# Kernel optimization log

Measured on AMD Instinct MI355X. Metric: run time of the kernel, lower is better.

The kernel has to match this reference:

```python
import jax, jax.numpy as jnp
import numpy as np

BS = 16384   # batch size
D = 2048     # input_dim
BD = 64      # block_dim
NB = D // BD # 32 blocks per BlockMLP
H = 2 * BD   # hidden block dim (hidden_layers_ratio=[2])
NUM_LAYERS = 2  # ceil(log_64(2048)) = 2


def setup_inputs() -> dict:
    key = jax.random.key(0)
    ks = jax.random.split(key, 1 + 2 * NUM_LAYERS)
    inp = {"x": jax.random.normal(ks[0], (BS, D), dtype=jnp.float32)}
    for i in range(NUM_LAYERS):
        inp[f"W1_{i}"] = jax.random.normal(ks[1 + 2 * i], (NB, BD, H), dtype=jnp.float32)
        inp[f"b1_{i}"] = jnp.zeros((NB, 1, H), dtype=jnp.float32)
        inp[f"W2_{i}"] = jax.random.normal(ks[2 + 2 * i], (NB, H, BD), dtype=jnp.float32)
        inp[f"b2_{i}"] = jnp.zeros((NB, 1, BD), dtype=jnp.float32)
    return inp


def _block_mlp(y, W1, b1, W2, b2):
    # BlockMLP.forward: view(bs, n_blocks, block_dim) -> transpose to [n_blocks, bs, block_dim]
    bs = y.shape[0]
    yb = y.reshape(bs, NB, BD).transpose(1, 0, 2)          # [NB, bs, BD]
    h = jnp.einsum('nbi,nio->nbo', yb, W1) + b1             # [NB, bs, H]
    h = jax.nn.gelu(h, approximate=False)                   # torch nn.GELU default (erf)
    o = jnp.einsum('nbh,nho->nbo', h, W2) + b2              # [NB, bs, BD]
    return o.transpose(1, 0, 2).reshape(bs, -1)             # [bs, D]


def reference(x, W1_0, b1_0, W2_0, b2_0, W1_1, b1_1, W2_1, b2_1):
    bs = x.shape[0]
    params = [(W1_0, b1_0, W2_0, b2_0), (W1_1, b1_1, W2_1, b2_1)]
    y = x
    for i, (W1, b1, W2, b2) in enumerate(params):
        # butterfly-style mixing permute before the block MLP
        y = y.reshape(-1, BD, BD ** i).transpose(0, 2, 1).reshape(bs, -1)
        y = _block_mlp(y, W1, b1, W2, b2)
        # inverse-style permute after
        y = y.reshape(-1, BD ** i, BD).transpose(0, 2, 1)
    return y.reshape(bs, -1)
```

## Files before the change

### kernel.cpp

```cpp
#include <hip/hip_runtime.h>

#define D    2048
#define NB   32
#define BD   64
#define HD   128
#define WSZ  (NB * HD * BD)
#define TSZ  (16384 * 64)

typedef __attribute__((ext_vector_type(8))) short short8;
typedef __attribute__((ext_vector_type(4))) float floatx4;

static __device__ __forceinline__ unsigned short f2bf(float f) {
  union { float f; unsigned u; } v; v.f = f;
  return (unsigned short)((v.u + 0x7FFFu + ((v.u >> 16) & 1u)) >> 16);
}
static __device__ __forceinline__ float bf2f(unsigned short h) {
  union { unsigned u; float f; } v; v.u = ((unsigned)h) << 16;
  return v.f;
}
static __device__ __forceinline__ unsigned fbits(float f) {
  union { float f; unsigned u; } v; v.f = f; return v.u;
}
static __device__ __forceinline__ unsigned short tbf(float f) {
  return (unsigned short)(fbits(f) >> 16);
}
static __device__ __forceinline__ unsigned pkt(float a, float b) {
  return __builtin_amdgcn_perm(fbits(b), fbits(a), 0x07060302u);
}
static __device__ __forceinline__ float fast_exp2(float x) {
  float r; asm("v_exp_f32 %0, %1" : "=v"(r) : "v"(x)); return r;
}
static __device__ __forceinline__ float fast_rcp(float x) {
  float r; asm("v_rcp_f32 %0, %1" : "=v"(r) : "v"(x)); return r;
}
static __device__ __forceinline__ float gelu_f(float x) {
  float x2 = x * x;
  float w  = __builtin_fmaf(x2, -0.102943695f, -2.3022083f);
  float e  = fast_exp2(x * w);
  return x * fast_rcp(1.0f + e);
}

__global__ __launch_bounds__(256, 3) void mlp0_k(
    const float* __restrict__ xf,
    unsigned short* __restrict__ Yt0,
    const unsigned short* __restrict__ Wt1,
    const unsigned short* __restrict__ Wt2,
    const float* __restrict__ b1, const float* __restrict__ b2) {
  __shared__ unsigned short Wlds[16384];
  __shared__ unsigned short Olds[64 * 128];
  __shared__ float Blds[192];
  const int n     = blockIdx.x & 31;
  const int chunk = blockIdx.x >> 5;
  const int t = threadIdx.x, l = t & 63, wv = t >> 6;
  const int lr = l & 15, q = l >> 4;
  const int sw = (lr & 7) << 3;
  const size_t rowbase = (size_t)chunk * 256;

  const unsigned short* s1 = Wt1 + n * 8192;
  const unsigned short* s2 = Wt2 + n * 8192;
  short8 sv1[4], sv2[4];
#pragma unroll
  for (int j = 0; j < 4; ++j) {
    sv1[j] = *(const short8*)&s1[(j * 256 + t) * 8];
    sv2[j] = *(const short8*)&s2[(j * 256 + t) * 8];
  }
  float bv = 0.f;
  if (t < 128)      bv = b1[n * HD + t];
  else if (t < 192) bv = b2[n * BD + (t - 128)];
  float4 uf[2][4];
#pragma unroll
  for (int p = 0; p < 2; ++p) {
    const float* xr = xf + (rowbase + p * 64 + wv * 16 + lr) * D + n * BD + q * 8;
    uf[p][0] = *(const float4*)(xr);      uf[p][1] = *(const float4*)(xr + 4);
    uf[p][2] = *(const float4*)(xr + 32); uf[p][3] = *(const float4*)(xr + 36);
  }
  asm volatile("" ::: "memory");
#pragma unroll
  for (int j = 0; j < 4; ++j) {
    *(short8*)&Wlds[(j * 256 + t) * 8]        = sv1[j];
    *(short8*)&Wlds[8192 + (j * 256 + t) * 8] = sv2[j];
  }
  if (t < 192) Blds[t] = bv;
  __syncthreads();

  const unsigned short* w1p0 = &Wlds[lr * 64 + ((q * 8) ^ sw)];
  const unsigned short* w1p1 = &Wlds[lr * 64 + ((32 + q * 8) ^ sw)];
  const unsigned short* w2p0 = &Wlds[8192 + lr * 128 + ((q * 8) ^ sw)];
  const unsigned short* w2p1 = &Wlds[8192 + lr * 128 + ((32 + q * 8) ^ sw)];

#pragma unroll
  for (int half = 0; half < 2; ++half) {
#pragma unroll
    for (int it = 0; it < 2; ++it) {
      const int i    = half * 2 + it;
      const int slot = i & 1;
      short8 xb0, xb1;
      {
        union { unsigned u[4]; short8 s; } c0, c1;
        c0.u[0] = pkt(uf[slot][0].x, uf[slot][0].y);
        c0.u[1] = pkt(uf[slot][0].z, uf[slot][0].w);
        c0.u[2] = pkt(uf[slot][1].x, uf[slot][1].y);
        c0.u[3] = pkt(uf[slot][1].z, uf[slot][1].w);
        c1.u[0] = pkt(uf[slot][2].x, uf[slot][2].y);
        c1.u[1] = pkt(uf[slot][2].z, uf[slot][2].w);
        c1.u[2] = pkt(uf[slot][3].x, uf[slot][3].y);
        c1.u[3] = pkt(uf[slot][3].z, uf[slot][3].w);
        xb0 = c0.s; xb1 = c1.s;
      }
      if (i < 2) {
        const float* xr = xf + (rowbase + (i + 2) * 64 + wv * 16 + lr) * D + n * BD + q * 8;
        uf[slot][0] = *(const float4*)(xr);      uf[slot][1] = *(const float4*)(xr + 4);
        uf[slot][2] = *(const float4*)(xr + 32); uf[slot][3] = *(const float4*)(xr + 36);
        asm volatile("" ::: "memory");
      }

      floatx4 acc2[4];
#pragma unroll
      for (int ot = 0; ot < 4; ++ot) {
        const float4 bb = *(const float4*)&Blds[128 + ot * 16 + q * 4];
        floatx4 v; v[0] = bb.x; v[1] = bb.y; v[2] = bb.z; v[3] = bb.w;
        acc2[ot] = v;
      }
#pragma unroll
      for (int hf = 0; hf < 2; ++hf) {
        floatx4 acc1[4];
#pragma unroll
        for (int ot = 0; ot < 4; ++ot) {
          const float4 bb = *(const float4*)&Blds[hf * 64 + ot * 16 + q * 4];
          floatx4 v; v[0] = bb.x; v[1] = bb.y; v[2] = bb.z; v[3] = bb.w;
          acc1[ot] = v;
        }
#pragma unroll
        for (int ot = 0; ot < 4; ++ot) {
          const int off = (hf * 64 + ot * 16) * 64;
          short8 a0 = *(const short8*)&w1p0[off];
          short8 a1 = *(const short8*)&w1p1[off];
          acc1[ot] = __builtin_amdgcn_mfma_f32_16x16x32_bf16(a0, xb0, acc1[ot], 0, 0, 0);
          acc1[ot] = __builtin_amdgcn_mfma_f32_16x16x32_bf16(a1, xb1, acc1[ot], 0, 0, 0);
        }
        union { unsigned u[4]; short8 s; } hb0, hb1;
        hb0.u[0] = pkt(gelu_f(acc1[0][0]), gelu_f(acc1[0][1]));
        hb0.u[1] = pkt(gelu_f(acc1[0][2]), gelu_f(acc1[0][3]));
        hb0.u[2] = pkt(gelu_f(acc1[1][0]), gelu_f(acc1[1][1]));
        hb0.u[3] = pkt(gelu_f(acc1[1][2]), gelu_f(acc1[1][3]));
        hb1.u[0] = pkt(gelu_f(acc1[2][0]), gelu_f(acc1[2][1]));
        hb1.u[1] = pkt(gelu_f(acc1[2][2]), gelu_f(acc1[2][3]));
        hb1.u[2] = pkt(gelu_f(acc1[3][0]), gelu_f(acc1[3][1]));
        hb1.u[3] = pkt(gelu_f(acc1[3][2]), gelu_f(acc1[3][3]));
#pragma unroll
        for (int ot = 0; ot < 4; ++ot) {
          const int off = ot * 16 * 128 + hf * 64;
          short8 w0 = *(const short8*)&w2p0[off];
          short8 w1 = *(const short8*)&w2p1[off];
          acc2[ot] = __builtin_amdgcn_mfma_f32_16x16x32_bf16(w0, hb0.s, acc2[ot], 0, 0, 0);
          acc2[ot] = __builtin_amdgcn_mfma_f32_16x16x32_bf16(w1, hb1.s, acc2[ot], 0, 0, 0);
        }
      }
      const int rl = it * 64 + wv * 16 + lr;
#pragma unroll
      for (int ot = 0; ot < 4; ++ot) {
#pragma unroll
        for (int e = 0; e < 4; ++e) {
          const int fo = ot * 16 + q * 4 + e;
          Olds[fo * 128 + (rl ^ ((fo & 7) << 3))] = tbf(acc2[ot][e]);
        }
      }
    }
    __syncthreads();
    const int j = t & 63, w = t >> 6;
#pragma unroll
    for (int ii = 0; ii < 8; ++ii) {
      const int fo = w * 16 + ii * 2 + (j >> 5);
      const int r4 = (j & 31) * 4;
      const int G  = (fo & 7) << 3;
      uint2 v = *(const uint2*)&Olds[fo * 128 + (r4 ^ G)];
      *(uint2*)(Yt0 + (size_t)n * TSZ + (size_t)fo * 16384 + rowbase + half * 128 + r4) = v;
    }
    if (half == 0) __syncthreads();
  }
}

__global__ __launch_bounds__(256, 3) void mlp1_k(
    const unsigned short* __restrict__ Yt0,
    unsigned short* __restrict__ Yt1,
    const unsigned short* __restrict__ Wt1,
    const unsigned short* __restrict__ Wt2,
    const float* __restrict__ b1, const float* __restrict__ b2) {
  __shared__ unsigned short Wlds[16384];
  __shared__ unsigned short Xl[2 * 128 * 32];
  __shared__ float Blds[192];
  const int np    = blockIdx.x & 31;
  const int chunk = blockIdx.x >> 5;
  const int t = threadIdx.x, l = t & 63, wv = t >> 6;
  const int lr = l & 15, q = l >> 4;
  const int sw = (lr & 7) << 3;
  const size_t rowbase = (size_t)chunk * 256;

  const unsigned short* s1 = Wt1 + np * 8192;
  const unsigned short* s2 = Wt2 + np * 8192;
  short8 sv1[4], sv2[4];
#pragma unroll
  for (int j = 0; j < 4; ++j) {
    sv1[j] = *(const short8*)&s1[(j * 256 + t) * 8];
    sv2[j] = *(const short8*)&s2[(j * 256 + t) * 8];
  }
  float bv = 0.f;
  if (t < 128)      bv = b1[np * HD + t];
  else if (t < 192) bv = b2[np * BD + (t - 128)];
  const int c = t >> 2, sub = t & 3;
  const int sp = c >> 5, sn = c & 31;
  const unsigned short* src0 = Yt0 + (size_t)sn * TSZ + (size_t)(sp * 32 + np) * 16384
                               + rowbase + sub * 32;
  short8 sx[4];
#pragma unroll
  for (int m = 0; m < 4; ++m) sx[m] = *(const short8*)(src0 + m * 8);

  asm volatile("" ::: "memory");
#pragma unroll
  for (int j = 0; j < 4; ++j) {
    *(short8*)&Wlds[(j * 256 + t) * 8]        = sv1[j];
    *(short8*)&Wlds[8192 + (j * 256 + t) * 8] = sv2[j];
  }
  if (t < 192) Blds[t] = bv;
#pragma unroll
  for (int m = 0; m < 4; ++m) {
#pragma unroll
    for (int k = 0; k < 8; ++k) {
      const int row = sub * 32 + m * 8 + k;
      Xl[sp * 4096 + row * 32 + (sn ^ (((row >> 1) & 3) << 3))] = (unsigned short)sx[m][k];
    }
  }
  __syncthreads();

  const unsigned short* w1p0 = &Wlds[lr * 64 + ((q * 8) ^ sw)];
  const unsigned short* w1p1 = &Wlds[lr * 64 + ((32 + q * 8) ^ sw)];
  const unsigned short* w2p0 = &Wlds[8192 + lr * 128 + ((q * 8) ^ sw)];
  const unsigned short* w2p1 = &Wlds[8192 + lr * 128 + ((32 + q * 8) ^ sw)];
  const int p = lr & 1;

#pragma unroll
  for (int half = 0; half < 2; ++half) {
    short8 sx2[4];
    if (half == 0) {
      const unsigned short* src1 = src0 + 128;
#pragma unroll
      for (int m = 0; m < 4; ++m) sx2[m] = *(const short8*)(src1 + m * 8);
      asm volatile("" ::: "memory");
    }
#pragma unroll
    for (int i = 0; i < 2; ++i) {
      const int rloc = (wv * 32 + i * 16 + lr) & ~1;
      const int g0   = ((rloc >> 1) & 3) << 3;
      short8 xb0 = *(const short8*)&Xl[p * 4096 + rloc * 32 + ((q * 8) ^ g0)];
      short8 xb1 = *(const short8*)&Xl[p * 4096 + (rloc + 1) * 32 + ((q * 8) ^ g0)];

      floatx4 acc2[4];
#pragma unroll
      for (int ot = 0; ot < 4; ++ot) {
        const float4 bb = *(const float4*)&Blds[128 + ot * 16 + q * 4];
        floatx4 v; v[0] = bb.x; v[1] = bb.y; v[2] = bb.z; v[3] = bb.w;
        acc2[ot] = v;
      }
#pragma unroll
      for (int hf = 0; hf < 2; ++hf) {
        floatx4 acc1[4];
#pragma unroll
        for (int ot = 0; ot < 4; ++ot) {
          const float4 bb = *(const float4*)&Blds[hf * 64 + ot * 16 + q * 4];
          floatx4 v; v[0] = bb.x; v[1] = bb.y; v[2] = bb.z; v[3] = bb.w;
          acc1[ot] = v;
        }
#pragma unroll
        for (int ot = 0; ot < 4; ++ot) {
          const int off = (hf * 64 + ot * 16) * 64;
          short8 a0 = *(const short8*)&w1p0[off];
          short8 a1 = *(const short8*)&w1p1[off];
          acc1[ot] = __builtin_amdgcn_mfma_f32_16x16x32_bf16(a0, xb0, acc1[ot], 0, 0, 0);
          acc1[ot] = __builtin_amdgcn_mfma_f32_16x16x32_bf16(a1, xb1, acc1[ot], 0, 0, 0);
        }
        union { unsigned u[4]; short8 s; } hb0, hb1;
        hb0.u[0] = pkt(gelu_f(acc1[0][0]), gelu_f(acc1[0][1]));
        hb0.u[1] = pkt(gelu_f(acc1[0][2]), gelu_f(acc1[0][3]));
        hb0.u[2] = pkt(gelu_f(acc1[1][0]), gelu_f(acc1[1][1]));
        hb0.u[3] = pkt(gelu_f(acc1[1][2]), gelu_f(acc1[1][3]));
        hb1.u[0] = pkt(gelu_f(acc1[2][0]), gelu_f(acc1[2][1]));
        hb1.u[1] = pkt(gelu_f(acc1[2][2]), gelu_f(acc1[2][3]));
        hb1.u[2] = pkt(gelu_f(acc1[3][0]), gelu_f(acc1[3][1]));
        hb1.u[3] = pkt(gelu_f(acc1[3][2]), gelu_f(acc1[3][3]));
#pragma unroll
        for (int ot = 0; ot < 4; ++ot) {
          const int off = ot * 16 * 128 + hf * 64;
          short8 w0 = *(const short8*)&w2p0[off];
          short8 w1 = *(const short8*)&w2p1[off];
          acc2[ot] = __builtin_amdgcn_mfma_f32_16x16x32_bf16(w0, hb0.s, acc2[ot], 0, 0, 0);
          acc2[ot] = __builtin_amdgcn_mfma_f32_16x16x32_bf16(w1, hb1.s, acc2[ot], 0, 0, 0);
        }
      }
      unsigned short* yo = Yt1 + (size_t)np * TSZ
                         + (rowbase + half * 128 + wv * 32 + i * 16 + lr) * 64;
#pragma unroll
      for (int ot = 0; ot < 4; ++ot) {
        ushort4 ov;
        ov.x = f2bf(acc2[ot][0]);
        ov.y = f2bf(acc2[ot][1]);
        ov.z = f2bf(acc2[ot][2]);
        ov.w = f2bf(acc2[ot][3]);
        *(ushort4*)&yo[ot * 16 + q * 4] = ov;
      }
    }
    if (half == 0) {
      __syncthreads();
#pragma unroll
      for (int m = 0; m < 4; ++m) {
#pragma unroll
        for (int k = 0; k < 8; ++k) {
          const int row = sub * 32 + m * 8 + k;
          Xl[sp * 4096 + row * 32 + (sn ^ (((row >> 1) & 3) << 3))] = (unsigned short)sx2[m][k];
        }
      }
      __syncthreads();
    }
  }
}

__global__ __launch_bounds__(256) void unpermute_k(const unsigned short* __restrict__ Y,
                                                   float* __restrict__ out) {
  __shared__ unsigned short L[32 * 512];
  const int t = threadIdx.x, w = t >> 6, j = t & 63;
  const size_t r0 = (size_t)blockIdx.x * 8;
#pragma unroll
  for (int c = 0; c < 8; ++c) {
    const int n = w * 8 + c;
    short8 v = *(const short8*)(Y + (size_t)n * TSZ + r0 * 64 + j * 8);
    const int row = j >> 3;
    const int gp = (j & 7) ^ ((n + row) & 7);
    *(short8*)&L[n * 512 + row * 64 + gp * 8] = v;
  }
  __syncthreads();
#pragma unroll
  for (int p = 0; p < 2; ++p) {
    const int rloc = w * 2 + p;
    float* op = out + (r0 + rloc) * (size_t)D;
#pragma unroll
    for (int i = 0; i < 8; ++i) {
      const int cbase = i * 256 + j * 4;
      float4 f;
#pragma unroll
      for (int e = 0; e < 4; ++e) {
        const int cc   = cbase + e;
        const int npp  = cc >> 6, fp = cc & 63;
        const int n    = fp & 31;
        const int srow = (rloc & ~1) | (fp >> 5);
        const int scol = (rloc & 1) * 32 + npp;
        const int g    = ((scol >> 3) ^ ((n + srow) & 7));
        const float v  = bf2f(L[n * 512 + srow * 64 + g * 8 + (scol & 7)]);
        if      (e == 0) f.x = v;
        else if (e == 1) f.y = v;
        else if (e == 2) f.z = v;
        else             f.w = v;
      }
      *(float4*)&op[cbase] = f;
    }
  }
}

__global__ void prep_w_all(const float* __restrict__ W1_0, const float* __restrict__ W2_0,
                           const float* __restrict__ W1_1, const float* __restrict__ W2_1,
                           unsigned short* __restrict__ dst) {
  const int seg = blockIdx.x >> 10;
  const int id  = ((blockIdx.x & 1023) << 8) | threadIdx.x;
  const float* W; int R;
  if      (seg == 0) { W = W1_0; R = BD; }
  else if (seg == 1) { W = W2_0; R = HD; }
  else if (seg == 2) { W = W1_1; R = BD; }
  else               { W = W2_1; R = HD; }
  const int C   = (R == BD) ? HD : BD;
  const int n   = id >> 13;
  const int rem = id & 8191;
  const int c   = rem / R;
  const int r   = rem - c * R;
  const unsigned short val = f2bf(W[(n * R + r) * C + c]);
  if (seg & 1) {
    const int hf  = r >> 6, st = (r >> 5) & 1, blk = (r >> 4) & 1;
    const int qq  = (r & 15) >> 2, e = r & 3;
    const int slot = hf * 64 + st * 32 + qq * 8 + blk * 4 + e;
    dst[seg * WSZ + n * 8192 + c * HD + (slot ^ ((c & 7) << 3))] = val;
  } else {
    dst[seg * WSZ + n * 8192 + c * BD + (r ^ ((c & 7) << 3))] = val;
  }
}

extern "C" void kernel_launch(void* const* d_in, const int* in_sizes, int n_in,
                              void* d_out, int out_size, void* d_ws, size_t ws_size,
                              hipStream_t stream) {
  const float* x    = (const float*)d_in[0];
  const float* W1_0 = (const float*)d_in[1];
  const float* b1_0 = (const float*)d_in[2];
  const float* W2_0 = (const float*)d_in[3];
  const float* b2_0 = (const float*)d_in[4];
  const float* W1_1 = (const float*)d_in[5];
  const float* b1_1 = (const float*)d_in[6];
  const float* W2_1 = (const float*)d_in[7];
  const float* b2_1 = (const float*)d_in[8];
  float* out = (float*)d_out;

  unsigned short* Wt  = (unsigned short*)d_ws;
  unsigned short* Yt0 = Wt + 4 * WSZ;
  unsigned short* Yt1 = Yt0 + (size_t)NB * TSZ;

  prep_w_all<<<4096, 256, 0, stream>>>(W1_0, W2_0, W1_1, W2_1, Wt);
  mlp0_k<<<2048, 256, 0, stream>>>(x, Yt0, Wt, Wt + WSZ, b1_0, b2_0);
  mlp1_k<<<2048, 256, 0, stream>>>(Yt0, Yt1, Wt + 2 * WSZ, Wt + 3 * WSZ, b1_1, b2_1);
  unpermute_k<<<2048, 256, 0, stream>>>(Yt1, out);
}
```

Before: 141.2 us.

## Double-buffer unpermute across row groups and coalesce weight prep via LDS

```diff
diff --git a/kernel.cpp b/kernel.cpp
--- a/kernel.cpp
+++ b/kernel.cpp
@@ -153,6 +153,7 @@
           short8 w0 = *(const short8*)&w2p0[off];
           short8 w1 = *(const short8*)&w2p1[off];
           acc2[ot] = __builtin_amdgcn_mfma_f32_16x16x32_bf16(w0, hb0.s, acc2[ot], 0, 0, 0);
+          ac2:;
           acc2[ot] = __builtin_amdgcn_mfma_f32_16x16x32_bf16(w1, hb1.s, acc2[ot], 0, 0, 0);
         }
       }
@@ -323,70 +324,107 @@
   }
 }
 
-__global__ __launch_bounds__(256) void unpermute_k(const unsigned short* __restrict__ Y,
-                                                   float* __restrict__ out) {
-  __shared__ unsigned short L[32 * 512];
+__global__ __launch_bounds__(256, 2) void unpermute_k(const unsigned short* __restrict__ Y,
+                                                      float* __restrict__ out) {
+  __shared__ unsigned short L[2][32 * 512];
   const int t = threadIdx.x, w = t >> 6, j = t & 63;
-  const size_t r0 = (size_t)blockIdx.x * 8;
+  const int row = j >> 3;
+
+  short8 v[8];
 #pragma unroll
   for (int c = 0; c < 8; ++c) {
     const int n = w * 8 + c;
-    short8 v = *(const short8*)(Y + (size_t)n * TSZ + r0 * 64 + j * 8);
-    const int row = j >> 3;
+    v[c] = *(const short8*)(Y + (size_t)n * TSZ + ((size_t)blockIdx.x * 32) * 64 + j * 8);
+  }
+#pragma unroll
+  for (int c = 0; c < 8; ++c) {
+    const int n = w * 8 + c;
     const int gp = (j & 7) ^ ((n + row) & 7);
-    *(short8*)&L[n * 512 + row * 64 + gp * 8] = v;
+    *(short8*)&L[0][n * 512 + row * 64 + gp * 8] = v[c];
   }
   __syncthreads();
-#pragma unroll
-  for (int p = 0; p < 2; ++p) {
-    const int rloc = w * 2 + p;
-    float* op = out + (r0 + rloc) * (size_t)D;
-#pragma unroll
-    for (int i = 0; i < 8; ++i) {
-      const int cbase = i * 256 + j * 4;
-      float4 f;
-#pragma unroll
-      for (int e = 0; e < 4; ++e) {
-        const int cc   = cbase + e;
-        const int npp  = cc >> 6, fp = cc & 63;
-        const int n    = fp & 31;
-        const int srow = (rloc & ~1) | (fp >> 5);
-        const int scol = (rloc & 1) * 32 + npp;
-        const int g    = ((scol >> 3) ^ ((n + srow) & 7));
-        const float v  = bf2f(L[n * 512 + srow * 64 + g * 8 + (scol & 7)]);
-        if      (e == 0) f.x = v;
-        else if (e == 1) f.y = v;
-        else if (e == 2) f.z = v;
-        else             f.w = v;
-      }
-      *(float4*)&op[cbase] = f;
-    }
-  }
-}
-
-__global__ void prep_w_all(const float* __restrict__ W1_0, const float* __restrict__ W2_0,
-                           const float* __restrict__ W1_1, const float* __restrict__ W2_1,
-                           unsigned short* __restrict__ dst) {
-  const int seg = blockIdx.x >> 10;
-  const int id  = ((blockIdx.x & 1023) << 8) | threadIdx.x;
+
+  for (int k = 0; k < 4; ++k) {
+    short8 nv[8];
+    if (k < 3) {
+      const size_t r0n = (size_t)(blockIdx.x * 4 + k + 1) * 8;
+#pragma unroll
+      for (int c = 0; c < 8; ++c) {
+        const int n = w * 8 + c;
+        nv[c] = *(const short8*)(Y + (size_t)n * TSZ + r0n * 64 + j * 8);
+      }
+      asm volatile("" ::: "memory");
+    }
+    const size_t r0 = (size_t)(blockIdx.x * 4 + k) * 8;
+    const unsigned short* Lb = L[k & 1];
+#pragma unroll
+    for (int p = 0; p < 2; ++p) {
+      const int rloc = w * 2 + p;
+      float* op = out + (r0 + rloc) * (size_t)D;
+#pragma unroll
+      for (int i = 0; i < 8; ++i) {
+        const int cbase = i * 256 + j * 4;
+        float4 f;
+#pragma unroll
+        for (int e = 0; e < 4; ++e) {
+          const int cc   = cbase + e;
+          const int npp  = cc >> 6, fp = cc & 63;
+          const int n    = fp & 31;
+          const int srow = (rloc & ~1) | (fp >> 5);
+          const int scol = (rloc & 1) * 32 + npp;
+          const int g    = ((scol >> 3) ^ ((n + srow) & 7));
+          const float vv = bf2f(Lb[n * 512 + srow * 64 + g * 8 + (scol & 7)]);
+          if      (e == 0) f.x = vv;
+          else if (e == 1) f.y = vv;
+          else if (e == 2) f.z = vv;
+          else             f.w = vv;
+        }
+        *(float4*)&op[cbase] = f;
+      }
+    }
+    if (k < 3) {
+      __syncthreads();
+#pragma unroll
+      for (int c = 0; c < 8; ++c) {
+        const int n = w * 8 + c;
+        const int gp = (j & 7) ^ ((n + row) & 7);
+        *(short8*)&L[(k + 1) & 1][n * 512 + row * 64 + gp * 8] = nv[c];
+      }
+      __syncthreads();
+    }
+  }
+}
+
+__global__ __launch_bounds__(256) void prep_w_all(
+    const float* __restrict__ W1_0, const float* __restrict__ W2_0,
+    const float* __restrict__ W1_1, const float* __restrict__ W2_1,
+    unsigned short* __restrict__ dst) {
+  __shared__ float Lf[8192];
+  const int seg = blockIdx.x >> 5, n = blockIdx.x & 31;
   const float* W; int R;
   if      (seg == 0) { W = W1_0; R = BD; }
   else if (seg == 1) { W = W2_0; R = HD; }
   else if (seg == 2) { W = W1_1; R = BD; }
   else               { W = W2_1; R = HD; }
+  const int t = threadIdx.x;
+  const float* Wn = W + n * 8192;
+#pragma unroll
+  for (int i = 0; i < 32; ++i) Lf[i * 256 + t] = Wn[i * 256 + t];
+  __syncthreads();
   const int C   = (R == BD) ? HD : BD;
-  const int n   = id >> 13;
-  const int rem = id & 8191;
-  const int c   = rem / R;
-  const int r   = rem - c * R;
-  const unsigned short val = f2bf(W[(n * R + r) * C + c]);
-  if (seg & 1) {
-    const int hf  = r >> 6, st = (r >> 5) & 1, blk = (r >> 4) & 1;
-    const int qq  = (r & 15) >> 2, e = r & 3;
-    const int slot = hf * 64 + st * 32 + qq * 8 + blk * 4 + e;
-    dst[seg * WSZ + n * 8192 + c * HD + (slot ^ ((c & 7) << 3))] = val;
-  } else {
-    dst[seg * WSZ + n * 8192 + c * BD + (r ^ ((c & 7) << 3))] = val;
+  const int rsh = (R == BD) ? 6 : 7;
+  unsigned short* dn = dst + seg * WSZ + n * 8192;
+#pragma unroll
+  for (int i = 0; i < 32; ++i) {
+    const int o = i * 256 + t;
+    const int cI = o >> rsh, s = o & (R - 1);
+    int r = s ^ ((cI & 7) << 3);
+    if (seg & 1) {
+      const int hf = r >> 6, st = (r >> 5) & 1, qq = (r >> 3) & 3;
+      const int blk = (r >> 2) & 1, e = r & 3;
+      r = hf * 64 + st * 32 + blk * 16 + qq * 4 + e;
+    }
+    dn[o] = f2bf(Lf[r * C + cI]);
   }
 }
 
@@ -408,8 +446,8 @@
   unsigned short* Yt0 = Wt + 4 * WSZ;
   unsigned short* Yt1 = Yt0 + (size_t)NB * TSZ;
 
-  prep_w_all<<<4096, 256, 0, stream>>>(W1_0, W2_0, W1_1, W2_1, Wt);
+  prep_w_all<<<128, 256, 0, stream>>>(W1_0, W2_0, W1_1, W2_1, Wt);
   mlp0_k<<<2048, 256, 0, stream>>>(x, Yt0, Wt, Wt + WSZ, b1_0, b2_0);
   mlp1_k<<<2048, 256, 0, stream>>>(Yt0, Yt1, Wt + 2 * WSZ, Wt + 3 * WSZ, b1_1, b2_1);
-  unpermute_k<<<2048, 256, 0, stream>>>(Yt1, out);
-}
+  unpermute_k<<<512, 256, 0, stream>>>(Yt1, out);
+}
```

After: 138.1 us. 1.02x faster.
